# Optimization experiments

Hardware: AMD Instinct MI355X
Metric: run time of the kernel (lower is better)

Reference implementation:

```python
import jax, jax.numpy as jnp
import numpy as np

B, N, D, H = 4, 1024, 1024, 16
NP = N - 1  # prototypes; +1 CLS slot -> n_valid == N
HD = D // H
LN_EPS = 1e-5


def _build_spatial_sim(key):
    centers = jax.random.uniform(key, (NP, 2), dtype=jnp.float32) * 10.0
    diff = centers[:, None, :] - centers[None, :, :]
    d2 = jnp.sum(diff * diff, axis=-1)           # squared pairwise distance
    dist = jnp.sqrt(d2)
    sigma = dist.mean()                           # spatial_sigma = mean cdist
    sim = jnp.exp(-d2 / (2.0 * sigma * sigma))
    sim = sim / sim.max()
    ext = jnp.zeros((NP + 1, NP + 1), dtype=jnp.float32)
    ext = ext.at[0, :].set(1.0).at[:, 0].set(1.0).at[1:, 1:].set(sim)
    return ext


def setup_inputs() -> dict:
    key = jax.random.key(0)
    kc, kx, kq, kp = jax.random.split(key, 4)
    spatial_sim = _build_spatial_sim(kc)          # [N, N] buffer
    x = jax.random.normal(kx, (B, N, D), dtype=jnp.float32)
    gamma = jnp.ones((D,), dtype=jnp.float32)
    beta = jnp.zeros((D,), dtype=jnp.float32)
    w_qkv = jax.random.normal(kq, (D, 3 * D), dtype=jnp.float32) * 0.02
    w_proj = jax.random.normal(kp, (D, D), dtype=jnp.float32) * 0.02
    b_proj = jnp.zeros((D,), dtype=jnp.float32)
    swl = jnp.float32(np.log(0.3 / 0.7))          # inverse_sigmoid(0.3)
    return {"x": x, "gamma": gamma, "beta": beta, "w_qkv": w_qkv,
            "w_proj": w_proj, "b_proj": b_proj,
            "spatial_weight_logit": swl, "spatial_sim": spatial_sim}


def reference(x, gamma, beta, w_qkv, w_proj, b_proj, spatial_weight_logit, spatial_sim):
    b, n, d = x.shape
    scale = HD ** (-0.5)
    # LayerNorm (biased variance, eps=1e-5)
    mu = x.mean(axis=-1, keepdims=True)
    var = jnp.mean((x - mu) ** 2, axis=-1, keepdims=True)
    x_norm = (x - mu) / jnp.sqrt(var + LN_EPS) * gamma + beta
    # QKV projection -> [B, H, N, HD] each
    qkv = (x_norm @ w_qkv).reshape(b, n, 3, H, HD)
    qkv = jnp.transpose(qkv, (2, 0, 3, 1, 4))
    q, k, v = qkv[0], qkv[1], qkv[2]
    scores = jnp.einsum('bhnd,bhmd->bhnm', q, k) * scale
    alpha = jax.nn.sigmoid(spatial_weight_logit)
    # blend feature attention with fixed spatial similarity, then softmax
    attn = jax.nn.softmax((1.0 - alpha) * scores + alpha * spatial_sim[None, None], axis=-1)
    out = jnp.einsum('bhnm,bhmd->bhnd', attn, v)
    out = jnp.transpose(out, (0, 2, 1, 3)).reshape(b, n, d)
    out = out @ w_proj + b_proj
    return x + out
```

## Files before the change

kernel.cpp:

```cpp
#include <hip/hip_runtime.h>

#define Bz 4
#define Nn 1024
#define Dd 1024
#define Hh 16
#define HD 64
#define SCALE 0.125f
#define LN_EPS 1e-5f

typedef __attribute__((ext_vector_type(8))) __bf16 bf16x8;
typedef __attribute__((ext_vector_type(4))) float f32x4;

static __device__ inline unsigned short f2bf(float f) {
    unsigned int u = __float_as_uint(f);
    u += 0x7fffu + ((u >> 16) & 1u);
    return (unsigned short)(u >> 16);
}

static __device__ inline bf16x8 ldfrag(const unsigned short* p) {
    return *(const bf16x8*)p;
}

static __device__ __forceinline__ void glds16(const unsigned short* g, unsigned short* l) {
    __builtin_amdgcn_global_load_lds((const __attribute__((address_space(1))) void*)g,
                                     (__attribute__((address_space(3))) void*)l, 16, 0, 0);
}

__global__ __launch_bounds__(256) void prep_kernel(const float* __restrict__ x,
                                                   const float* __restrict__ gamma,
                                                   const float* __restrict__ beta,
                                                   unsigned short* __restrict__ xn,
                                                   const float* __restrict__ w_qkv,
                                                   unsigned short* __restrict__ wqkvT,
                                                   const float* __restrict__ w_proj,
                                                   unsigned short* __restrict__ wprojT) {
    __shared__ float tile[32][33];
    int blk = blockIdx.x;
    int tid = threadIdx.x;

    if (blk < 4096) {
        const float* xr = x + (size_t)blk * Dd;
        float4 v = ((const float4*)xr)[tid];
        float s = v.x + v.y + v.z + v.w;
        float ss = v.x * v.x + v.y * v.y + v.z * v.z + v.w * v.w;
        for (int o = 32; o > 0; o >>= 1) {
            s += __shfl_down(s, o);
            ss += __shfl_down(ss, o);
        }
        float* red = &tile[0][0];
        int wid = tid >> 6;
        if ((tid & 63) == 0) { red[wid * 2] = s; red[wid * 2 + 1] = ss; }
        __syncthreads();
        float tot = red[0] + red[2] + red[4] + red[6];
        float tot2 = red[1] + red[3] + red[5] + red[7];
        float mu = tot * (1.0f / Dd);
        float var = tot2 * (1.0f / Dd) - mu * mu;
        float inv = rsqrtf(var + LN_EPS);
        float4 g = ((const float4*)gamma)[tid];
        float4 b = ((const float4*)beta)[tid];
        ushort4 o4;
        o4.x = f2bf((v.x - mu) * inv * g.x + b.x);
        o4.y = f2bf((v.y - mu) * inv * g.y + b.y);
        o4.z = f2bf((v.z - mu) * inv * g.z + b.z);
        o4.w = f2bf((v.w - mu) * inv * g.w + b.w);
        ((ushort4*)(xn + (size_t)blk * Dd))[tid] = o4;
    } else {
        const float* in;
        unsigned short* out;
        int cols, c0, r0;
        if (blk < 7168) {
            int idx = blk - 4096;
            in = w_qkv; out = wqkvT; cols = 3072;
            c0 = (idx % 96) * 32; r0 = (idx / 96) * 32;
        } else {
            int idx = blk - 7168;
            in = w_proj; out = wprojT; cols = 1024;
            c0 = (idx % 32) * 32; r0 = (idx / 32) * 32;
        }
        int tx = tid & 31, ty = tid >> 5;
        #pragma unroll
        for (int i = 0; i < 32; i += 8)
            tile[ty + i][tx] = in[(size_t)(r0 + ty + i) * cols + c0 + tx];
        __syncthreads();
        #pragma unroll
        for (int i = 0; i < 32; i += 8)
            out[(size_t)(c0 + ty + i) * 1024 + r0 + tx] = f2bf(tile[tx][ty + i]);
    }
}


__global__ __launch_bounds__(256) void gemm_qkv(const unsigned short* __restrict__ A,
                                                const unsigned short* __restrict__ Bt,
                                                unsigned short* __restrict__ qb,
                                                unsigned short* __restrict__ kb,
                                                unsigned short* __restrict__ vtb) {
    __shared__ unsigned short sA[8192], sB[8192];
    int tid = threadIdx.x;
    int w = tid >> 6, lane = tid & 63, lrow = lane & 15, quad = lane >> 4;
    int wm = w >> 1, wn = w & 1;
    int rowbase = blockIdx.y * 128;
    int colbase = blockIdx.x * 128;

    int srow = tid >> 3;
    int gch = ((tid & 7) - (srow >> 1)) & 7;
    const unsigned short* gA = A + (size_t)(rowbase + srow) * 1024 + gch * 8;
    const unsigned short* gB = Bt + (size_t)(colbase + srow) * 1024 + gch * 8;
    unsigned short* lA = sA + w * 512;
    unsigned short* lB = sB + w * 512;

    int bs0 = ((quad + (lrow >> 1)) & 7) * 8;
    int bs1 = ((4 + quad + (lrow >> 1)) & 7) * 8;
    const unsigned short* fa = sA + (wm * 64 + lrow) * 64;
    const unsigned short* fb = sB + (wn * 64 + lrow) * 64;

    f32x4 acc[4][4];
    #pragma unroll
    for (int i = 0; i < 4; i++)
        #pragma unroll
        for (int j = 0; j < 4; j++)
            acc[i][j] = (f32x4){0.f, 0.f, 0.f, 0.f};

    for (int k0 = 0; k0 < 1024; k0 += 64) {
        __syncthreads();
        #pragma unroll
        for (int c = 0; c < 4; c++) {
            glds16(gA + (size_t)c * 32768 + k0, lA + c * 2048);
            glds16(gB + (size_t)c * 32768 + k0, lB + c * 2048);
        }
        __syncthreads();
        #pragma unroll
        for (int s = 0; s < 2; s++) {
            int bo = s ? bs1 : bs0;
            bf16x8 a[4], b[4];
            #pragma unroll
            for (int i = 0; i < 4; i++) a[i] = *(const bf16x8*)(fa + i * 1024 + bo);
            #pragma unroll
            for (int j = 0; j < 4; j++) b[j] = *(const bf16x8*)(fb + j * 1024 + bo);
            #pragma unroll
            for (int i = 0; i < 4; i++)
                #pragma unroll
                for (int j = 0; j < 4; j++)
                    acc[i][j] = __builtin_amdgcn_mfma_f32_16x16x32_bf16(a[i], b[j], acc[i][j], 0, 0, 0);
        }
    }

    if (colbase < 2048) {
        #pragma unroll
        for (int j = 0; j < 4; j++) {
            int col = colbase + wn * 64 + j * 16 + lrow;
            int s = col >> 10, rem = col & 1023;
            int h = rem >> 6, e = rem & 63;
            unsigned short* dst = (s == 0) ? qb : kb;
            #pragma unroll
            for (int i = 0; i < 4; i++) {
                #pragma unroll
                for (int r = 0; r < 4; r++) {
                    int R = rowbase + wm * 64 + i * 16 + quad * 4 + r;
                    int bb = R >> 10, n = R & 1023;
                    dst[(((size_t)(bb * Hh + h)) * Nn + n) * HD + e] = f2bf(acc[i][j][r]);
                }
            }
        }
    } else {
        int bb = rowbase >> 10;
        int nbase = (rowbase & 1023) + wm * 64;
        unsigned short* sc = sA + w * 2048;
        int er = lane >> 2, nc = lane & 3;
        #pragma unroll
        for (int j = 0; j < 4; j++) {
            __syncthreads();
            int ebase = colbase + wn * 64 + j * 16 - 2048;
            int h = ebase >> 6, e0 = ebase & 63;
            #pragma unroll
            for (int i = 0; i < 4; i++) {
                uint2 pk;
                pk.x = (unsigned)f2bf(acc[i][j][0]) | ((unsigned)f2bf(acc[i][j][1]) << 16);
                pk.y = (unsigned)f2bf(acc[i][j][2]) | ((unsigned)f2bf(acc[i][j][3]) << 16);
                *(uint2*)(sc + lrow * 68 + i * 16 + quad * 4) = pk;
            }
            __syncthreads();
            unsigned short* vrow = vtb + ((size_t)((bb * Hh + h) * HD) + e0 + er) * Nn + nbase;
            #pragma unroll
            for (int c = 0; c < 4; c++) {
                uint2 v = *(const uint2*)(sc + er * 68 + c * 16 + nc * 4);
                *(uint2*)(vrow + c * 16 + nc * 4) = v;
            }
        }
    }
}

__global__ __launch_bounds__(256) void gemm_proj(const unsigned short* __restrict__ A,
                                                 const unsigned short* __restrict__ Bt,
                                                 const float* __restrict__ bias,
                                                 const float* __restrict__ x,
                                                 float* __restrict__ out) {
    __shared__ unsigned short sA[8192], sB[8192];
    int tid = threadIdx.x;
    int w = tid >> 6, lane = tid & 63, lrow = lane & 15, quad = lane >> 4;
    int wm = w >> 1, wn = w & 1;
    int rowbase = blockIdx.y * 128;
    int colbase = blockIdx.x * 128;

    int srow = tid >> 3;
    int gch = ((tid & 7) - (srow >> 1)) & 7;
    const unsigned short* gA = A + (size_t)(rowbase + srow) * 1024 + gch * 8;
    const unsigned short* gB = Bt + (size_t)(colbase + srow) * 1024 + gch * 8;
    unsigned short* lA = sA + w * 512;
    unsigned short* lB = sB + w * 512;

    int bs0 = ((quad + (lrow >> 1)) & 7) * 8;
    int bs1 = ((4 + quad + (lrow >> 1)) & 7) * 8;
    const unsigned short* fa = sA + (wm * 64 + lrow) * 64;
    const unsigned short* fb = sB + (wn * 64 + lrow) * 64;

    f32x4 acc[4][4];
    #pragma unroll
    for (int i = 0; i < 4; i++)
        #pragma unroll
        for (int j = 0; j < 4; j++)
            acc[i][j] = (f32x4){0.f, 0.f, 0.f, 0.f};

    for (int k0 = 0; k0 < 1024; k0 += 64) {
        __syncthreads();
        #pragma unroll
        for (int c = 0; c < 4; c++) {
            glds16(gA + (size_t)c * 32768 + k0, lA + c * 2048);
            glds16(gB + (size_t)c * 32768 + k0, lB + c * 2048);
        }
        __syncthreads();
        #pragma unroll
        for (int s = 0; s < 2; s++) {
            int bo = s ? bs1 : bs0;
            bf16x8 a[4], b[4];
            #pragma unroll
            for (int i = 0; i < 4; i++) a[i] = *(const bf16x8*)(fa + i * 1024 + bo);
            #pragma unroll
            for (int j = 0; j < 4; j++) b[j] = *(const bf16x8*)(fb + j * 1024 + bo);
            #pragma unroll
            for (int i = 0; i < 4; i++)
                #pragma unroll
                for (int j = 0; j < 4; j++)
                    acc[i][j] = __builtin_amdgcn_mfma_f32_16x16x32_bf16(a[i], b[j], acc[i][j], 0, 0, 0);
        }
    }

    #pragma unroll
    for (int j = 0; j < 4; j++) {
        int col = colbase + wn * 64 + j * 16 + lrow;
        float bc = bias[col];
        #pragma unroll
        for (int i = 0; i < 4; i++) {
            #pragma unroll
            for (int r = 0; r < 4; r++) {
                int R = rowbase + wm * 64 + i * 16 + quad * 4 + r;
                out[(size_t)R * 1024 + col] = acc[i][j][r] + bc + x[(size_t)R * 1024 + col];
            }
        }
    }
}

#define PSTR 72
#define LOG2E 1.4426950408889634f
__global__ __launch_bounds__(256, 2) void attn_kernel(const unsigned short* __restrict__ qb,
                                                      const unsigned short* __restrict__ kb,
                                                      const unsigned short* __restrict__ vtb,
                                                      const float* __restrict__ sim,
                                                      const float* __restrict__ swl,
                                                      unsigned short* __restrict__ aout) {
    int h = blockIdx.y, bb = blockIdx.z;
    int n0 = blockIdx.x * 128;
    int tid = threadIdx.x;
    int w = tid >> 6, lane = tid & 63;
    int lrow = lane & 15, quad = lane >> 4;
    const unsigned short* q = qb + ((size_t)(bb * Hh + h)) * Nn * HD;
    const unsigned short* k = kb + ((size_t)(bb * Hh + h)) * Nn * HD;
    const unsigned short* vt = vtb + ((size_t)(bb * Hh + h)) * HD * Nn;
    float alpha = 1.f / (1.f + __expf(-swl[0]));
    float c1 = (1.f - alpha) * SCALE * LOG2E;
    float a2 = alpha * LOG2E;

    __shared__ unsigned short sK[2][4096];
    __shared__ unsigned short sP[128 * PSTR];

    int qr0 = n0 + w * 32;
    bf16x8 qf[2][2];
    #pragma unroll
    for (int g = 0; g < 2; g++) {
        qf[g][0] = ldfrag(q + (size_t)(qr0 + g * 16 + lrow) * HD + quad * 8);
        qf[g][1] = ldfrag(q + (size_t)(qr0 + g * 16 + lrow) * HD + 32 + quad * 8);
    }

    f32x4 o[2][4];
    #pragma unroll
    for (int g = 0; g < 2; g++)
        #pragma unroll
        for (int et = 0; et < 4; et++) o[g][et] = (f32x4){0.f, 0.f, 0.f, 0.f};
    float rsum[2] = {0.f, 0.f};

    int bs0 = (quad + (lrow >> 1)) & 7;
    int bs1 = (4 + quad + (lrow >> 1)) & 7;
    unsigned short* sPw = sP + (w * 32) * PSTR;

    int c0i = tid, c1i = 256 + tid;
    int row0 = c0i >> 3, cg0 = ((c0i & 7) - (row0 >> 1)) & 7;
    int row1 = c1i >> 3, cg1 = ((c1i & 7) - (row1 >> 1)) & 7;
    const unsigned short* gK0 = k + (size_t)row0 * HD + cg0 * 8;
    const unsigned short* gK1 = k + (size_t)row1 * HD + cg1 * 8;
    const float* gS0 = sim + (size_t)(qr0 + lrow) * Nn + quad * 4;
    const float* gS1 = gS0 + (size_t)16 * Nn;

    glds16(gK0, &sK[0][0] + tid * 8);
    glds16(gK1, &sK[0][0] + 2048 + tid * 8);
    float4 sm[4][2];
    #pragma unroll
    for (int ks = 0; ks < 4; ks++) {
        sm[ks][0] = *(const float4*)(gS0 + ks * 16);
        sm[ks][1] = *(const float4*)(gS1 + ks * 16);
    }
    __syncthreads();

    for (int t = 0; t < 16; t++) {
        int cur = t & 1;
        int m0 = t * 64;

        bf16x8 vreg[2][4];
        #pragma unroll
        for (int ms = 0; ms < 2; ms++)
            #pragma unroll
            for (int et = 0; et < 4; et++) {
                int e = et * 16 + lrow;
                vreg[ms][et] = *(const bf16x8*)(vt + (size_t)e * Nn + m0 + ms * 32 + quad * 8);
            }

        float4 smN[4][2];
        if (t < 15) {
            int m1 = m0 + 64;
            unsigned short* dst = &sK[cur ^ 1][0];
            glds16(gK0 + (size_t)m1 * HD, dst + tid * 8);
            glds16(gK1 + (size_t)m1 * HD, dst + 2048 + tid * 8);
            #pragma unroll
            for (int ks = 0; ks < 4; ks++) {
                smN[ks][0] = *(const float4*)(gS0 + m1 + ks * 16);
                smN[ks][1] = *(const float4*)(gS1 + m1 + ks * 16);
            }
        }

        const unsigned short* sKc = sK[cur];
        #pragma unroll
        for (int ks = 0; ks < 4; ks++) {
            const unsigned short* kr = sKc + (ks * 16 + lrow) * 64;
            bf16x8 ak0 = *(const bf16x8*)(kr + bs0 * 8);
            bf16x8 ak1 = *(const bf16x8*)(kr + bs1 * 8);
            #pragma unroll
            for (int g = 0; g < 2; g++) {
                f32x4 c = (f32x4){0.f, 0.f, 0.f, 0.f};
                c = __builtin_amdgcn_mfma_f32_16x16x32_bf16(ak0, qf[g][0], c, 0, 0, 0);
                c = __builtin_amdgcn_mfma_f32_16x16x32_bf16(ak1, qf[g][1], c, 0, 0, 0);
                float e0 = __builtin_amdgcn_exp2f(c1 * c[0] + a2 * sm[ks][g].x);
                float e1 = __builtin_amdgcn_exp2f(c1 * c[1] + a2 * sm[ks][g].y);
                float e2 = __builtin_amdgcn_exp2f(c1 * c[2] + a2 * sm[ks][g].z);
                float e3 = __builtin_amdgcn_exp2f(c1 * c[3] + a2 * sm[ks][g].w);
                rsum[g] += (e0 + e1) + (e2 + e3);
                uint2 pk;
                pk.x = (__float_as_uint(e0) >> 16) | (__float_as_uint(e1) & 0xffff0000u);
                pk.y = (__float_as_uint(e2) >> 16) | (__float_as_uint(e3) & 0xffff0000u);
                *(uint2*)(sPw + (g * 16 + lrow) * PSTR + ks * 16 + quad * 4) = pk;
            }
        }

        __builtin_amdgcn_s_setprio(1);
        #pragma unroll
        for (int ms = 0; ms < 2; ms++) {
            bf16x8 pa[2];
            #pragma unroll
            for (int g = 0; g < 2; g++)
                pa[g] = *(const bf16x8*)(sPw + (g * 16 + lrow) * PSTR + ms * 32 + quad * 8);
            #pragma unroll
            for (int et = 0; et < 4; et++)
                #pragma unroll
                for (int g = 0; g < 2; g++)
                    o[g][et] = __builtin_amdgcn_mfma_f32_16x16x32_bf16(pa[g], vreg[ms][et], o[g][et], 0, 0, 0);
        }
        __builtin_amdgcn_s_setprio(0);

        __syncthreads();
        if (t < 15) {
            #pragma unroll
            for (int ks = 0; ks < 4; ks++) {
                sm[ks][0] = smN[ks][0];
                sm[ks][1] = smN[ks][1];
            }
        }
    }

    #pragma unroll
    for (int g = 0; g < 2; g++) {
        rsum[g] += __shfl_xor(rsum[g], 16);
        rsum[g] += __shfl_xor(rsum[g], 32);
    }

    #pragma unroll
    for (int g = 0; g < 2; g++)
        #pragma unroll
        for (int r = 0; r < 4; r++) {
            float inv = 1.f / __shfl(rsum[g], quad * 4 + r);
            int qn = qr0 + g * 16 + quad * 4 + r;
            #pragma unroll
            for (int et = 0; et < 4; et++)
                aout[((size_t)bb * Nn + qn) * Dd + h * HD + et * 16 + lrow]
                    = f2bf(o[g][et][r] * inv);
        }
}

extern "C" void kernel_launch(void* const* d_in, const int* in_sizes, int n_in,
                              void* d_out, int out_size, void* d_ws, size_t ws_size,
                              hipStream_t stream) {
    const float* x      = (const float*)d_in[0];
    const float* gamma  = (const float*)d_in[1];
    const float* beta   = (const float*)d_in[2];
    const float* w_qkv  = (const float*)d_in[3];
    const float* w_proj = (const float*)d_in[4];
    const float* b_proj = (const float*)d_in[5];
    const float* swl    = (const float*)d_in[6];
    const float* sim    = (const float*)d_in[7];
    float* out = (float*)d_out;

    unsigned short* ws = (unsigned short*)d_ws;
    unsigned short* xn     = ws;
    unsigned short* wqkvT  = xn + 4194304;
    unsigned short* wprojT = wqkvT + 3145728;
    unsigned short* qb     = wprojT + 1048576;
    unsigned short* kb     = qb + 4194304;
    unsigned short* vtb    = kb + 4194304;
    unsigned short* aout   = vtb + 4194304;

    prep_kernel<<<8192, 256, 0, stream>>>(x, gamma, beta, xn, w_qkv, wqkvT, w_proj, wprojT);
    gemm_qkv<<<dim3(24, 32), 256, 0, stream>>>(xn, wqkvT, qb, kb, vtb);
    attn_kernel<<<dim3(8, 16, 4), 256, 0, stream>>>(qb, kb, vtb, sim, swl, aout);
    gemm_proj<<<dim3(8, 32), 256, 0, stream>>>(aout, wprojT, b_proj, x, out);
}
```

Measured before the change: 215.5 us.

## Stage V tiles through double-buffered LDS and swizzle the P buffer

V^T tiles are now loaded with async global-to-LDS copies into a double buffer alongside K, instead of each wave reading them directly from global into registers every iteration. The P scratch buffer drops its padded stride in favour of an XOR swizzle to avoid bank conflicts. This cuts redundant global V reads across the four waves and hides their latency behind compute, at the cost of more LDS use (which may affect occupancy at two blocks per CU).

After: 202.0 us. 1.07x faster.

```diff
diff --git a/kernel.cpp b/kernel.cpp
--- a/kernel.cpp
+++ b/kernel.cpp
@@ -259,7 +259,6 @@
     }
 }
 
-#define PSTR 72
 #define LOG2E 1.4426950408889634f
 __global__ __launch_bounds__(256, 2) void attn_kernel(const unsigned short* __restrict__ qb,
                                                       const unsigned short* __restrict__ kb,
@@ -280,7 +279,8 @@
     float a2 = alpha * LOG2E;
 
     __shared__ unsigned short sK[2][4096];
-    __shared__ unsigned short sP[128 * PSTR];
+    __shared__ unsigned short sV[2][4096];
+    __shared__ unsigned short sP[8192];
 
     int qr0 = n0 + w * 32;
     bf16x8 qf[2][2];
@@ -299,18 +299,19 @@
 
     int bs0 = (quad + (lrow >> 1)) & 7;
     int bs1 = (4 + quad + (lrow >> 1)) & 7;
-    unsigned short* sPw = sP + (w * 32) * PSTR;
-
-    int c0i = tid, c1i = 256 + tid;
-    int row0 = c0i >> 3, cg0 = ((c0i & 7) - (row0 >> 1)) & 7;
-    int row1 = c1i >> 3, cg1 = ((c1i & 7) - (row1 >> 1)) & 7;
-    const unsigned short* gK0 = k + (size_t)row0 * HD + cg0 * 8;
-    const unsigned short* gK1 = k + (size_t)row1 * HD + cg1 * 8;
+    unsigned short* sPw = sP + (w * 32) * 64;
+
     const float* gS0 = sim + (size_t)(qr0 + lrow) * Nn + quad * 4;
     const float* gS1 = gS0 + (size_t)16 * Nn;
 
-    glds16(gK0, &sK[0][0] + tid * 8);
-    glds16(gK1, &sK[0][0] + 2048 + tid * 8);
+    #pragma unroll
+    for (int i = 0; i < 2; i++) {
+        int slot = i * 256 + tid;
+        int row = slot >> 3;
+        int cg = ((slot & 7) - (row >> 1)) & 7;
+        glds16(k + (size_t)row * HD + cg * 8, &sK[0][0] + i * 2048 + w * 512);
+        glds16(vt + (size_t)row * Nn + cg * 8, &sV[0][0] + i * 2048 + w * 512);
+    }
     float4 sm[4][2];
     #pragma unroll
     for (int ks = 0; ks < 4; ks++) {
@@ -321,23 +322,17 @@
 
     for (int t = 0; t < 16; t++) {
         int cur = t & 1;
-        int m0 = t * 64;
-
-        bf16x8 vreg[2][4];
-        #pragma unroll
-        for (int ms = 0; ms < 2; ms++)
-            #pragma unroll
-            for (int et = 0; et < 4; et++) {
-                int e = et * 16 + lrow;
-                vreg[ms][et] = *(const bf16x8*)(vt + (size_t)e * Nn + m0 + ms * 32 + quad * 8);
-            }
-
         float4 smN[4][2];
         if (t < 15) {
-            int m1 = m0 + 64;
-            unsigned short* dst = &sK[cur ^ 1][0];
-            glds16(gK0 + (size_t)m1 * HD, dst + tid * 8);
-            glds16(gK1 + (size_t)m1 * HD, dst + 2048 + tid * 8);
+            int m1 = (t + 1) * 64;
+            #pragma unroll
+            for (int i = 0; i < 2; i++) {
+                int slot = i * 256 + tid;
+                int row = slot >> 3;
+                int cg = ((slot & 7) - (row >> 1)) & 7;
+                glds16(k + (size_t)(m1 + row) * HD + cg * 8, &sK[cur ^ 1][0] + i * 2048 + w * 512);
+                glds16(vt + (size_t)row * Nn + m1 + cg * 8, &sV[cur ^ 1][0] + i * 2048 + w * 512);
+            }
             #pragma unroll
             for (int ks = 0; ks < 4; ks++) {
                 smN[ks][0] = *(const float4*)(gS0 + m1 + ks * 16);
@@ -346,6 +341,7 @@
         }
 
         const unsigned short* sKc = sK[cur];
+        const unsigned short* sVc = sV[cur];
         #pragma unroll
         for (int ks = 0; ks < 4; ks++) {
             const unsigned short* kr = sKc + (ks * 16 + lrow) * 64;
@@ -364,7 +360,9 @@
                 uint2 pk;
                 pk.x = (__float_as_uint(e0) >> 16) | (__float_as_uint(e1) & 0xffff0000u);
                 pk.y = (__float_as_uint(e2) >> 16) | (__float_as_uint(e3) & 0xffff0000u);
-                *(uint2*)(sPw + (g * 16 + lrow) * PSTR + ks * 16 + quad * 4) = pk;
+                int row = g * 16 + lrow;
+                int chv = (ks * 2 + (quad >> 1)) ^ (row & 7);
+                *(uint2*)(sPw + row * 64 + chv * 8 + (quad & 1) * 4) = pk;
             }
         }
 
@@ -373,13 +371,20 @@
         for (int ms = 0; ms < 2; ms++) {
             bf16x8 pa[2];
             #pragma unroll
-            for (int g = 0; g < 2; g++)
-                pa[g] = *(const bf16x8*)(sPw + (g * 16 + lrow) * PSTR + ms * 32 + quad * 8);
-            #pragma unroll
-            for (int et = 0; et < 4; et++)
+            for (int g = 0; g < 2; g++) {
+                int row = g * 16 + lrow;
+                int chp = (ms * 4 + quad) ^ (row & 7);
+                pa[g] = *(const bf16x8*)(sPw + row * 64 + chp * 8);
+            }
+            #pragma unroll
+            for (int et = 0; et < 4; et++) {
+                int e = et * 16 + lrow;
+                int slot = (ms * 4 + quad + (e >> 1)) & 7;
+                bf16x8 vb = *(const bf16x8*)(sVc + e * 64 + slot * 8);
                 #pragma unroll
                 for (int g = 0; g < 2; g++)
-                    o[g][et] = __builtin_amdgcn_mfma_f32_16x16x32_bf16(pa[g], vreg[ms][et], o[g][et], 0, 0, 0);
+                    o[g][et] = __builtin_amdgcn_mfma_f32_16x16x32_bf16(pa[g], vb, o[g][et], 0, 0, 0);
+            }
         }
         __builtin_amdgcn_s_setprio(0);
 
```
